# Kernel optimization log

Measured on AMD Instinct MI355X. Metric: run time of the kernel, lower is better.

The kernel has to match this reference:

```python
import jax, jax.numpy as jnp
import numpy as np

B, L, D, H, HD, FF, NL = 2, 2048, 1024, 16, 64, 4096, 2
EPS = 1e-5
NEG = -1e30


def setup_inputs() -> dict:
    key = jax.random.key(0)
    ks = jax.random.split(key, 20)
    x = jax.random.normal(ks[0], (B, L, D), jnp.float32)
    # RoPE tables, rotate-half convention: [L, HD]
    pos = jnp.arange(L, dtype=jnp.float32)
    freqs = 1.0 / (10000.0 ** (jnp.arange(0, HD, 2, dtype=jnp.float32) / HD))
    ang = pos[:, None] * freqs[None, :]              # [L, HD/2]
    cos = jnp.concatenate([jnp.cos(ang), jnp.cos(ang)], -1)
    sin = jnp.concatenate([jnp.sin(ang), jnp.sin(ang)], -1)
    s = 0.02
    wq = jax.random.normal(ks[1], (NL, D, D), jnp.float32) * s
    wk = jax.random.normal(ks[2], (NL, D, D), jnp.float32) * s
    wv = jax.random.normal(ks[3], (NL, D, D), jnp.float32) * s
    wo = jax.random.normal(ks[4], (NL, D, D), jnp.float32) * s
    w1 = jax.random.normal(ks[5], (NL, D, FF), jnp.float32) * s
    w2 = jax.random.normal(ks[6], (NL, FF, D), jnp.float32) * s
    w3 = jax.random.normal(ks[7], (NL, D, FF), jnp.float32) * s
    attn_norm = jnp.ones((NL, D), jnp.float32)
    mlp_norm = jnp.ones((NL, D), jnp.float32)
    final_norm = jnp.ones((D,), jnp.float32)
    rw1 = jax.random.normal(ks[8], (D, D), jnp.float32) * s
    rb1 = jnp.zeros((D,), jnp.float32)
    rw2 = jax.random.normal(ks[9], (D, 1), jnp.float32) * s
    rb2 = jnp.zeros((1,), jnp.float32)
    return dict(x=x, cos=cos, sin=sin, wq=wq, wk=wk, wv=wv, wo=wo,
                w1=w1, w2=w2, w3=w3, attn_norm=attn_norm, mlp_norm=mlp_norm,
                final_norm=final_norm, rw1=rw1, rb1=rb1, rw2=rw2, rb2=rb2)


def _rms(x, w):
    return x * jax.lax.rsqrt(jnp.mean(x * x, -1, keepdims=True) + EPS) * w


def _rope(t, cos, sin):
    # t: [B, L, H, HD]; cos/sin: [L, HD]
    t1, t2 = jnp.split(t, 2, axis=-1)
    rot = jnp.concatenate([-t2, t1], -1)
    return t * cos[None, :, None, :] + rot * sin[None, :, None, :]


def reference(x, cos, sin, wq, wk, wv, wo, w1, w2, w3,
              attn_norm, mlp_norm, final_norm, rw1, rb1, rw2, rb2):
    causal = jnp.tril(jnp.ones((L, L), bool))
    h = x
    for i in range(NL):  # small fixed layer loop
        a = _rms(h, attn_norm[i])
        q = _rope((a @ wq[i]).reshape(B, L, H, HD), cos, sin)
        k = _rope((a @ wk[i]).reshape(B, L, H, HD), cos, sin)
        v = (a @ wv[i]).reshape(B, L, H, HD)
        sc = jnp.einsum('bqhd,bkhd->bhqk', q, k) / np.float32(np.sqrt(HD))
        sc = jnp.where(causal, sc, NEG)
        o = jnp.einsum('bhqk,bkhd->bqhd', jax.nn.softmax(sc, -1), v)
        h = h + o.reshape(B, L, D) @ wo[i]
        m = _rms(h, mlp_norm[i])
        h = h + (jax.nn.silu(m @ w1[i]) * (m @ w3[i])) @ w2[i]
    h = _rms(h, final_norm)

    # router chunking: straight-through hard boundaries
    logits = (jax.nn.silu(h @ rw1 + rb1) @ rw2 + rb2)[..., 0]   # [B, L]
    probs = jax.nn.sigmoid(logits)
    hard = (probs > 0.5).astype(h.dtype)
    mask = probs + jax.lax.stop_gradient(hard - probs)
    mask = mask.at[:, 0].set(1.0)
    mhard = jax.lax.stop_gradient(mask)
    # select matrix: S padded to static upper bound L (rows >= counts are zero)
    cums = jnp.cumsum(mhard, -1)                                # [B, L]
    seg = jnp.arange(1, L + 1, dtype=cums.dtype)[None, :, None] # [1, S, 1]
    assignment = (cums[:, None, :] == seg).astype(h.dtype)      # [B, S, L]
    select = assignment * mask[:, None, :]
    compressed = jnp.einsum('bsl,bld->bsd', select, h)          # [B, S, D]
    boundary_positions = jnp.argsort(-mhard, axis=-1)           # stable in jax
    counts = mhard.sum(-1).astype(jnp.int32)
    avg_chunk_size = jnp.float32(L) / jnp.mean(counts.astype(jnp.float32))
    return (h, compressed, boundary_positions, counts, avg_chunk_size)
```

## Files before the change

### kernel.cpp

```cpp
#include <hip/hip_runtime.h>
#include <cmath>

#define B_  2
#define L_  2048
#define D_  1024
#define H_  16
#define FF_ 4096
#define NL_ 2
#define NT_ (B_*L_)
#define ND_ (NT_*D_)

typedef __attribute__((ext_vector_type(8))) short bf16x8;
typedef __attribute__((ext_vector_type(4))) float f32x4;

__device__ __forceinline__ short f2bf(float x){
  unsigned u = __builtin_bit_cast(unsigned, x);
  unsigned r = (u + 0x7fffu + ((u>>16)&1u)) >> 16;
  return (short)r;
}
__device__ __forceinline__ float bf2f(short s){
  unsigned u = ((unsigned)(unsigned short)s) << 16;
  return __builtin_bit_cast(float, u);
}
#define MFMA16(a,b,c) __builtin_amdgcn_mfma_f32_16x16x32_bf16(a,b,c,0,0,0)

__device__ __forceinline__ void gload16(const short* g, short* l){
  __builtin_amdgcn_global_load_lds((const __attribute__((address_space(1))) void*)g,
                                   (__attribute__((address_space(3))) void*)l, 16, 0, 0);
}

template<bool WF32>
__global__ __launch_bounds__(256) void k_rmsnorm_s(const float* __restrict__ in,
                                                   const float* __restrict__ w,
                                                   short* __restrict__ oh,
                                                   short* __restrict__ ol,
                                                   float* __restrict__ of){
  int row = blockIdx.x; int tid = threadIdx.x;
  float4 xv = ((const float4*)(in + (size_t)row*D_))[tid];
  float ss = xv.x*xv.x + xv.y*xv.y + xv.z*xv.z + xv.w*xv.w;
  #pragma unroll
  for (int off=32; off; off>>=1) ss += __shfl_xor(ss, off);
  __shared__ float wsum[4];
  if ((tid&63)==0) wsum[tid>>6] = ss;
  __syncthreads();
  float tot = wsum[0]+wsum[1]+wsum[2]+wsum[3];
  float scale = 1.0f / sqrtf(tot*(1.0f/(float)D_) + 1e-5f);
  float4 w4 = ((const float4*)w)[tid];
  float v[4] = {xv.x*scale*w4.x, xv.y*scale*w4.y, xv.z*scale*w4.z, xv.w*scale*w4.w};
  short4 hh, ll;
  short h0=f2bf(v[0]); hh.x=h0; ll.x=f2bf(v[0]-bf2f(h0));
  short h1=f2bf(v[1]); hh.y=h1; ll.y=f2bf(v[1]-bf2f(h1));
  short h2=f2bf(v[2]); hh.z=h2; ll.z=f2bf(v[2]-bf2f(h2));
  short h3=f2bf(v[3]); hh.w=h3; ll.w=f2bf(v[3]-bf2f(h3));
  *(short4*)(oh + (size_t)row*D_ + tid*4) = hh;
  *(short4*)(ol + (size_t)row*D_ + tid*4) = ll;
  if (WF32){
    float4 ov; ov.x=v[0]; ov.y=v[1]; ov.z=v[2]; ov.w=v[3];
    ((float4*)(of + (size_t)row*D_))[tid] = ov;
  }
}

__global__ __launch_bounds__(256) void k_wsplit(const float* __restrict__ src,
                                                short* __restrict__ dh,
                                                short* __restrict__ dl,
                                                int srcN, int kOff, int nOff, int KT){
  __shared__ float t[64][68];
  int k0 = blockIdx.x*64, n0v = blockIdx.y*64;
  int tid = threadIdx.x;
  #pragma unroll
  for (int p=0;p<4;p++){
    int r = p*16 + (tid>>4);
    int c4 = (tid&15)*4;
    float4 v = *(const float4*)(src + (size_t)(kOff + k0 + r)*srcN + nOff + n0v + c4);
    *(float4*)&t[r][c4] = v;
  }
  __syncthreads();
  int n = tid>>2, kk = (tid&3)*16;
  bf16x8 H0, L0, H1, L1;
  #pragma unroll
  for (int q=0;q<8;q++){
    float v = t[kk+q][n]; short h=f2bf(v); H0[q]=h; L0[q]=f2bf(v-bf2f(h));
  }
  #pragma unroll
  for (int q=0;q<8;q++){
    float v = t[kk+8+q][n]; short h=f2bf(v); H1[q]=h; L1[q]=f2bf(v-bf2f(h));
  }
  size_t dof = (size_t)(n0v + n)*KT + k0 + kk;
  *(bf16x8*)(dh + dof) = H0;  *(bf16x8*)(dh + dof + 8) = H1;
  *(bf16x8*)(dl + dof) = L0;  *(bf16x8*)(dl + dof + 8) = L1;
}

__global__ __launch_bounds__(256,2) void k_qkv_mm(const short* __restrict__ Ah,
                                                  const short* __restrict__ Al,
                                                  const short* __restrict__ Wh,
                                                  const short* __restrict__ Wl,
                                                  short* __restrict__ OutH){
  __shared__ short lds[32768];
  int tid = threadIdx.x, wid = tid>>6, lane = tid&63;
  int l15 = lane&15, l4 = lane>>4;
  int wr = wid>>1, wc = wid&1;
  int m0 = blockIdx.y*128, n0 = blockIdx.x*128;
  const int K = 1024;
  f32x4 acc[4][4];
  #pragma unroll
  for (int i=0;i<4;i++){
    #pragma unroll
    for (int j=0;j<4;j++) acc[i][j] = (f32x4){0.f,0.f,0.f,0.f};
  }
  const short* gsrc = (wid==0)?Ah:(wid==1)?Al:(wid==2)?Wh:Wl;
  int rb = (wid<2)? m0 : n0;
  int gcol = ((lane&7)^(lane>>3))*8;
  short* ldsw = lds + wid*8192;
  const short* gp0 = gsrc + (size_t)(rb + (lane>>3))*K + gcol;
  for (int k0=0; k0<K; k0+=64){
    const short* gp = gp0 + k0;
    #pragma unroll
    for (int lc=0; lc<16; ++lc)
      gload16(gp + (size_t)lc*8*K, ldsw + lc*512);
    __syncthreads();
    #pragma unroll
    for (int ks=0; ks<2; ++ks){
      bf16x8 af[4], alf[4], wf[4], wlf[4];
      int gs = ((ks*4 + l4) ^ (lane&7))*8;
      #pragma unroll
      for (int f=0; f<4; ++f){
        int ar = (wr*64 + f*16 + l15)*64 + gs;
        af[f]  = *(const bf16x8*)&lds[ar];
        alf[f] = *(const bf16x8*)&lds[8192 + ar];
        int wr2 = (wc*64 + f*16 + l15)*64 + gs;
        wf[f]  = *(const bf16x8*)&lds[16384 + wr2];
        wlf[f] = *(const bf16x8*)&lds[24576 + wr2];
      }
      #pragma unroll
      for (int i=0;i<4;i++){
        #pragma unroll
        for (int j=0;j<4;j++){
          acc[i][j] = MFMA16(af[i],  wf[j],  acc[i][j]);
          acc[i][j] = MFMA16(alf[i], wf[j],  acc[i][j]);
          acc[i][j] = MFMA16(af[i],  wlf[j], acc[i][j]);
        }
      }
    }
    __syncthreads();
  }
  int sel = n0 >> 10;
  short* oh = OutH + (size_t)sel*8388608;
  short* ol = oh + 4194304;
  int cb = (n0 & 1023) + wc*64;
  #pragma unroll
  for (int i=0;i<4;i++){
    #pragma unroll
    for (int j=0;j<4;j++){
      #pragma unroll
      for (int r=0;r<4;r++){
        size_t mg = (size_t)(m0 + wr*64 + i*16 + l4*4 + r);
        int ng = cb + j*16 + l15;
        float v = acc[i][j][r];
        short h = f2bf(v);
        oh[mg*1024 + ng] = h;
        ol[mg*1024 + ng] = f2bf(v - bf2f(h));
      }
    }
  }
}

template<int EPI>
__global__ __launch_bounds__(256,2) void k_mm64(const short* __restrict__ Ah,
                                                const short* __restrict__ Al,
                                                const short* __restrict__ Wh,
                                                const short* __restrict__ Wl,
                                                const short* __restrict__ W3h,
                                                const short* __restrict__ W3l,
                                                int K,
                                                float* __restrict__ Cf,
                                                const float* __restrict__ bias,
                                                short* __restrict__ Gh,
                                                short* __restrict__ Gl,
                                                int ldc){
  __shared__ short lds[(EPI==3)?32768:24576];
  int tid = threadIdx.x, wid = tid>>6, lane = tid&63;
  int l15 = lane&15, l4 = lane>>4;
  int m0 = blockIdx.y*128, n0 = blockIdx.x*64;
  f32x4 a1[2][4], a3[2][4];
  #pragma unroll
  for (int i=0;i<2;i++){
    #pragma unroll
    for (int j=0;j<4;j++){ a1[i][j]=(f32x4){0.f,0.f,0.f,0.f}; a3[i][j]=(f32x4){0.f,0.f,0.f,0.f}; }
  }
  int gcol = ((lane&7)^(lane>>3))*8;
  int l8 = lane>>3;
  const int NCH = (EPI==3)? 16 : 12;
  for (int k0=0; k0<K; k0+=64){
    for (int t=0; t<NCH; ++t){
      int c = wid*NCH + t;
      const short* sb; int row0; short* db;
      if (c < 32){
        sb = (c<16)? Ah : Al; row0 = m0 + (c&15)*8;
        db = lds + ((c<16)?0:8192) + (c&15)*512;
      } else {
        int wseg = (c-32)>>3;
        sb = (wseg==0)?Wh:(wseg==1)?Wl:(wseg==2)?W3h:W3l;
        row0 = n0 + (c&7)*8;
        db = lds + 16384 + wseg*4096 + (c&7)*512;
      }
      gload16(sb + (size_t)(row0 + l8)*K + k0 + gcol, db);
    }
    __syncthreads();
    #pragma unroll
    for (int ks=0; ks<2; ++ks){
      int gs = ((ks*4 + l4) ^ (lane&7))*8;
      bf16x8 af[2], alf[2], wh[4], wl[4];
      #pragma unroll
      for (int f=0; f<2; ++f){
        int ar = (wid*32 + f*16 + l15)*64 + gs;
        af[f]  = *(const bf16x8*)&lds[ar];
        alf[f] = *(const bf16x8*)&lds[8192 + ar];
      }
      #pragma unroll
      for (int f=0; f<4; ++f){
        int wr2 = (f*16 + l15)*64 + gs;
        wh[f] = *(const bf16x8*)&lds[16384 + wr2];
        wl[f] = *(const bf16x8*)&lds[20480 + wr2];
      }
      #pragma unroll
      for (int i=0;i<2;i++){
        #pragma unroll
        for (int j=0;j<4;j++){
          a1[i][j] = MFMA16(af[i],  wh[j], a1[i][j]);
          a1[i][j] = MFMA16(alf[i], wh[j], a1[i][j]);
          a1[i][j] = MFMA16(af[i],  wl[j], a1[i][j]);
        }
      }
      if (EPI==3){
        bf16x8 w3h[4], w3l[4];
        #pragma unroll
        for (int f=0; f<4; ++f){
          int wr2 = (f*16 + l15)*64 + gs;
          w3h[f] = *(const bf16x8*)&lds[24576 + wr2];
          w3l[f] = *(const bf16x8*)&lds[28672 + wr2];
        }
        #pragma unroll
        for (int i=0;i<2;i++){
          #pragma unroll
          for (int j=0;j<4;j++){
            a3[i][j] = MFMA16(af[i],  w3h[j], a3[i][j]);
            a3[i][j] = MFMA16(alf[i], w3h[j], a3[i][j]);
            a3[i][j] = MFMA16(af[i],  w3l[j], a3[i][j]);
          }
        }
      }
    }
    __syncthreads();
  }
  #pragma unroll
  for (int i=0;i<2;i++){
    #pragma unroll
    for (int j=0;j<4;j++){
      #pragma unroll
      for (int r=0;r<4;r++){
        size_t mg = (size_t)(m0 + wid*32 + i*16 + l4*4 + r);
        int ng = n0 + j*16 + l15;
        float v = a1[i][j][r];
        if (EPI==1){
          float* cp = Cf + mg*ldc + ng;
          *cp = *cp + v;
        } else if (EPI==2){
          float x = v + bias[ng];
          Cf[mg*ldc + ng] = x/(1.f+expf(-x));
        } else {
          float g = v/(1.f+expf(-v)) * a3[i][j][r];
          short h = f2bf(g);
          Gh[mg*2048 + ng] = h;
          Gl[mg*2048 + ng] = f2bf(g - bf2f(h));
        }
      }
    }
  }
}

__global__ __launch_bounds__(256) void k_prep_k(const short* __restrict__ kh,
                                                const short* __restrict__ kl,
                                                const float* __restrict__ cosT,
                                                const float* __restrict__ sinT,
                                                short* __restrict__ kf){
  int wave = threadIdx.x>>6, lane = threadIdx.x&63;
  int t16 = blockIdx.x*4 + wave;
  int bh = blockIdx.y; int b = bh>>4, h = bh&15;
  int l15 = lane&15, l4 = lane>>4;
  int tok = t16*16 + l15;
  const short* khp = kh + (size_t)(b*L_+tok)*D_ + h*64;
  const short* klp = kl + (size_t)(b*L_+tok)*D_ + h*64;
  int d0 = l4*8;
  bf16x8 ka  = *(const bf16x8*)(khp + d0);
  bf16x8 kb2 = *(const bf16x8*)(khp + 32 + d0);
  bf16x8 kla = *(const bf16x8*)(klp + d0);
  bf16x8 klb = *(const bf16x8*)(klp + 32 + d0);
  const float* cr = cosT + (size_t)tok*64;
  const float* sr = sinT + (size_t)tok*64;
  float c0[8], s0[8], c1[8], s1[8];
  *(float4*)&c0[0] = *(const float4*)(cr + d0);      *(float4*)&c0[4] = *(const float4*)(cr + d0 + 4);
  *(float4*)&c1[0] = *(const float4*)(cr + 32 + d0); *(float4*)&c1[4] = *(const float4*)(cr + 32 + d0 + 4);
  *(float4*)&s0[0] = *(const float4*)(sr + d0);      *(float4*)&s0[4] = *(const float4*)(sr + d0 + 4);
  *(float4*)&s1[0] = *(const float4*)(sr + 32 + d0); *(float4*)&s1[4] = *(const float4*)(sr + 32 + d0 + 4);
  bf16x8 h0, lo0, h1, lo1;
  #pragma unroll
  for (int j=0;j<8;j++){
    float k0v = bf2f(ka[j]) + bf2f(kla[j]);
    float k1v = bf2f(kb2[j]) + bf2f(klb[j]);
    float r0 = k0v*c0[j] - k1v*s0[j];
    float r1 = k1v*c1[j] + k0v*s1[j];
    short a = f2bf(r0); h0[j]=a; lo0[j]=f2bf(r0 - bf2f(a));
    short bS = f2bf(r1); h1[j]=bS; lo1[j]=f2bf(r1 - bf2f(bS));
  }
  size_t base = ((size_t)(bh*128 + t16)*4)*512 + lane*8;
  *(bf16x8*)(kf + base)        = h0;
  *(bf16x8*)(kf + base + 512)  = lo0;
  *(bf16x8*)(kf + base + 1024) = h1;
  *(bf16x8*)(kf + base + 1536) = lo1;
}

__global__ __launch_bounds__(256) void k_prep_v(const short* __restrict__ vh,
                                                const short* __restrict__ vl,
                                                short* __restrict__ vf){
  int wave = threadIdx.x>>6, lane = threadIdx.x&63;
  int kc = blockIdx.x;
  int bh = blockIdx.y; int b = bh>>4, h = bh&15;
  int dt = wave;
  int l15 = lane&15, l4 = lane>>4;
  bf16x8 hi, lo;
  #pragma unroll
  for (int i=0;i<8;i++){
    size_t off = (size_t)(b*L_ + kc*32 + l4*8 + i)*D_ + h*64 + dt*16 + l15;
    hi[i] = vh[off];
    lo[i] = vl[off];
  }
  size_t base = (((size_t)(bh*64 + kc)*4 + dt)*2)*512 + lane*8;
  *(bf16x8*)(vf + base)       = hi;
  *(bf16x8*)(vf + base + 512) = lo;
}

__global__ __launch_bounds__(256) void k_attn_mfma(const short* __restrict__ qhb,
                                                   const short* __restrict__ qlb,
                                                   const short* __restrict__ kf,
                                                   const short* __restrict__ vf,
                                                   const float* __restrict__ cosT,
                                                   const float* __restrict__ sinT,
                                                   short* __restrict__ oh,
                                                   short* __restrict__ ol){
  int qt = 31 - (int)blockIdx.x;
  int bh = blockIdx.y; int b = bh>>4, h = bh&15;
  int wave = threadIdx.x>>6, lane = threadIdx.x&63;
  int l15 = lane&15, l4 = lane>>4;
  __shared__ short pblob[4][2048];
  short* pb = pblob[wave];

  int tok = qt*64 + wave*16 + l15;
  const short* qhp = qhb + (size_t)(b*L_+tok)*D_ + h*64;
  const short* qlp = qlb + (size_t)(b*L_+tok)*D_ + h*64;
  int d0 = l4*8;
  bf16x8 qa  = *(const bf16x8*)(qhp + d0);
  bf16x8 qb2 = *(const bf16x8*)(qhp + 32 + d0);
  bf16x8 qla = *(const bf16x8*)(qlp + d0);
  bf16x8 qlb2= *(const bf16x8*)(qlp + 32 + d0);
  const float* cr = cosT + (size_t)tok*64;
  const float* sr = sinT + (size_t)tok*64;
  float c0[8], s0[8], c1[8], s1[8];
  *(float4*)&c0[0] = *(const float4*)(cr + d0);      *(float4*)&c0[4] = *(const float4*)(cr + d0 + 4);
  *(float4*)&c1[0] = *(const float4*)(cr + 32 + d0); *(float4*)&c1[4] = *(const float4*)(cr + 32 + d0 + 4);
  *(float4*)&s0[0] = *(const float4*)(sr + d0);      *(float4*)&s0[4] = *(const float4*)(sr + d0 + 4);
  *(float4*)&s1[0] = *(const float4*)(sr + 32 + d0); *(float4*)&s1[4] = *(const float4*)(sr + 32 + d0 + 4);
  bf16x8 qh0, ql0, qh1, ql1;
  #pragma unroll
  for (int j=0;j<8;j++){
    float q0v = bf2f(qa[j]) + bf2f(qla[j]);
    float q1v = bf2f(qb2[j]) + bf2f(qlb2[j]);
    float r0 = (q0v*c0[j] - q1v*s0[j]) * 0.125f;
    float r1 = (q1v*c1[j] + q0v*s1[j]) * 0.125f;
    short a = f2bf(r0); qh0[j]=a; ql0[j]=f2bf(r0 - bf2f(a));
    short bS = f2bf(r1); qh1[j]=bS; ql1[j]=f2bf(r1 - bf2f(bS));
  }

  f32x4 O[4];
  #pragma unroll
  for (int dt=0;dt<4;dt++) O[dt] = (f32x4){0.f,0.f,0.f,0.f};
  float m_[4] = {-1e30f,-1e30f,-1e30f,-1e30f};
  float ls[4] = {0.f,0.f,0.f,0.f};

  for (int kt=0; kt<=qt; ++kt){
    bool dtile = (kt == qt);
    f32x4 sr4[4];
    const short* kbase = kf + ((size_t)(bh*128 + kt*4)*4)*512 + lane*8;
    #pragma unroll
    for (int g=0; g<4; g++){
      f32x4 acc = (f32x4){0.f,0.f,0.f,0.f};
      if (!(dtile && g > wave)){
        const short* kp = kbase + (size_t)g*2048;
        bf16x8 kh0 = *(const bf16x8*)(kp);
        bf16x8 kl0 = *(const bf16x8*)(kp + 512);
        bf16x8 kh1 = *(const bf16x8*)(kp + 1024);
        bf16x8 kl1 = *(const bf16x8*)(kp + 1536);
        acc = MFMA16(qh0, kh0, acc); acc = MFMA16(qh1, kh1, acc);
        acc = MFMA16(ql0, kh0, acc); acc = MFMA16(ql1, kh1, acc);
        acc = MFMA16(qh0, kl0, acc); acc = MFMA16(qh1, kl1, acc);
      }
      sr4[g] = acc;
    }
    float p_[4][4];
    #pragma unroll
    for (int r=0; r<4; r++){
      int rowrel = wave*16 + l4*4 + r;
      float mx = -1e30f;
      float sv[4];
      #pragma unroll
      for (int g=0; g<4; g++){
        float v = sr4[g][r];
        if (dtile && (g*16 + l15) > rowrel) v = -1e30f;
        sv[g] = v; mx = fmaxf(mx, v);
      }
      #pragma unroll
      for (int off=1; off<16; off<<=1) mx = fmaxf(mx, __shfl_xor(mx, off));
      float nm = fmaxf(m_[r], mx);
      float al = __expf(m_[r] - nm);
      m_[r] = nm;
      float ps = 0.f;
      #pragma unroll
      for (int g=0; g<4; g++){ float pv = __expf(sv[g] - nm); p_[g][r] = pv; ps += pv; }
      #pragma unroll
      for (int off=1; off<16; off<<=1) ps += __shfl_xor(ps, off);
      ls[r] = ls[r]*al + ps;
      #pragma unroll
      for (int dt=0; dt<4; dt++) O[dt][r] *= al;
    }
    #pragma unroll
    for (int g=0; g<4; g++){
      int key = g*16 + l15;
      int cc = key>>5, sub = (key>>3)&3, ii = key&7;
      #pragma unroll
      for (int r=0; r<4; r++){
        float pv = p_[g][r];
        short ph = f2bf(pv);
        short pl = f2bf(pv - bf2f(ph));
        int idx = cc*1024 + (sub*16 + l4*4 + r)*8 + ii;
        pb[idx] = ph;
        pb[idx + 512] = pl;
      }
    }
    asm volatile("s_waitcnt lgkmcnt(0)" ::: "memory");
    const short* vbase = vf + ((size_t)(bh*64 + kt*2)*8)*512 + lane*8;
    #pragma unroll
    for (int cc=0; cc<2; cc++){
      bf16x8 pah = *(const bf16x8*)(pb + cc*1024 + lane*8);
      bf16x8 pal = *(const bf16x8*)(pb + cc*1024 + 512 + lane*8);
      #pragma unroll
      for (int dt=0; dt<4; dt++){
        const short* vp = vbase + (size_t)cc*4096 + dt*1024;
        bf16x8 vh = *(const bf16x8*)(vp);
        bf16x8 vl = *(const bf16x8*)(vp + 512);
        O[dt] = MFMA16(pah, vh, O[dt]);
        O[dt] = MFMA16(pal, vh, O[dt]);
        O[dt] = MFMA16(pah, vl, O[dt]);
      }
    }
  }
  #pragma unroll
  for (int r=0; r<4; r++){
    float inv = 1.0f / ls[r];
    size_t row = (size_t)(b*L_ + qt*64 + wave*16 + l4*4 + r);
    #pragma unroll
    for (int dt=0; dt<4; dt++){
      float v = O[dt][r]*inv;
      short hh = f2bf(v);
      oh[row*D_ + h*64 + dt*16 + l15] = hh;
      ol[row*D_ + h*64 + dt*16 + l15] = f2bf(v - bf2f(hh));
    }
  }
}

__global__ __launch_bounds__(256) void k_gemv(const float* __restrict__ T,
                                              const float* __restrict__ rw2,
                                              const float* __restrict__ rb2,
                                              float* __restrict__ logits){
  int row = blockIdx.x; int tid = threadIdx.x;
  float4 tv = ((const float4*)(T + (size_t)row*D_))[tid];
  float4 wv = ((const float4*)rw2)[tid];
  float s = tv.x*wv.x + tv.y*wv.y + tv.z*wv.z + tv.w*wv.w;
  #pragma unroll
  for (int off=32; off; off>>=1) s += __shfl_xor(s, off);
  __shared__ float ps[4];
  if ((tid&63)==0) ps[tid>>6] = s;
  __syncthreads();
  if (tid==0) logits[row] = ps[0]+ps[1]+ps[2]+ps[3] + rb2[0];
}

__global__ __launch_bounds__(256) void k_boundary(const float* __restrict__ logits,
                                                  float* __restrict__ pos_out,
                                                  int* __restrict__ hard,
                                                  int* __restrict__ cums,
                                                  int* __restrict__ counts){
  int b = blockIdx.x; int tid = threadIdx.x;
  __shared__ int part[256];
  int loc[8]; int s=0;
  int base = b*L_;
  #pragma unroll
  for (int j=0;j<8;j++){
    int ll = tid*8 + j;
    float lg = logits[base+ll];
    int hv = (ll==0) ? 1 : ((lg > 0.0f) ? 1 : 0);
    loc[j]=hv; s+=hv;
  }
  part[tid]=s; __syncthreads();
  for (int off=1; off<256; off<<=1){
    int v = part[tid];
    int add = (tid>=off) ? part[tid-off] : 0;
    __syncthreads();
    part[tid] = v + add;
    __syncthreads();
  }
  int total = part[255];
  int run = part[tid] - s;
  #pragma unroll
  for (int j=0;j<8;j++){
    int ll = tid*8+j;
    run += loc[j];
    hard[base+ll] = loc[j];
    cums[base+ll] = run;
    int idx = loc[j] ? (run-1) : (total + ll - run);
    pos_out[base+idx] = (float)ll;
  }
  if (tid==0) counts[b] = total;
}

__global__ __launch_bounds__(256) void k_scatter(const float* __restrict__ hf,
                                                 const int* __restrict__ hard,
                                                 const int* __restrict__ cums,
                                                 float* __restrict__ comp){
  int rowid = blockIdx.x;
  if (!hard[rowid]) return;
  int b = rowid >> 11;
  int s = cums[rowid]-1;
  const float4* src = (const float4*)(hf + (size_t)rowid*D_);
  float4* dst = (float4*)(comp + (size_t)(b*L_ + s)*D_);
  dst[threadIdx.x] = src[threadIdx.x];
}

__global__ void k_finalize(const int* __restrict__ counts, float* __restrict__ out){
  if (threadIdx.x==0 && blockIdx.x==0){
    float c0 = (float)counts[0], c1 = (float)counts[1];
    out[0]=c0; out[1]=c1;
    out[2] = (float)L_ / (0.5f*(c0+c1));
  }
}

extern "C" void kernel_launch(void* const* d_in, const int* in_sizes, int n_in,
                              void* d_out, int out_size, void* d_ws, size_t ws_size,
                              hipStream_t stream){
  const float* x      = (const float*)d_in[0];
  const float* cosT   = (const float*)d_in[1];
  const float* sinT   = (const float*)d_in[2];
  const float* wq     = (const float*)d_in[3];
  const float* wk     = (const float*)d_in[4];
  const float* wv     = (const float*)d_in[5];
  const float* wo     = (const float*)d_in[6];
  const float* w1     = (const float*)d_in[7];
  const float* w2     = (const float*)d_in[8];
  const float* w3     = (const float*)d_in[9];
  const float* attn_n = (const float*)d_in[10];
  const float* mlp_n  = (const float*)d_in[11];
  const float* final_n= (const float*)d_in[12];
  const float* rw1    = (const float*)d_in[13];
  const float* rb1    = (const float*)d_in[14];
  const float* rw2    = (const float*)d_in[15];
  const float* rb2    = (const float*)d_in[16];

  float* outF = (float*)d_out;
  float* hD   = outF;
  float* compD= outF + (size_t)ND_;
  float* posD = outF + (size_t)2*ND_;

  char* WS = (char*)d_ws;
  auto S = [&](size_t mb){ return (short*)(WS + mb*1048576ull); };
  auto F = [&](size_t mb){ return (float*)(WS + mb*1048576ull); };
  short *ah=S(0), *al=S(8);
  short *qh=S(16), *ql=S(24), *kh=S(32), *kl=S(40), *vh=S(48), *vl=S(56);
  short *qkvwt_h=S(64), *qkvwt_l=S(70);
  short *vf=S(64);
  short *kf=S(48);
  short *wot_h=S(32), *wot_l=S(34);
  short *gh=S(16), *gl=S(32);
  short *w1t_h=S(48), *w1t_l=S(52), *w3t_h=S(56), *w3t_l=S(60);
  short *w2t_h=S(64), *w2t_l=S(68);
  short *rw1t_h=S(16), *rw1t_l=S(18);
  float *ra=F(20);
  float *logits=F(76);
  int *hard=(int*)(logits+NT_), *cums=hard+NT_, *cnts=cums+NT_;
  short *oh=(short*)compD, *ol=oh+4194304;

  hipMemcpyAsync(hD, x, (size_t)ND_*sizeof(float), hipMemcpyDeviceToDevice, stream);

  for (int i=0;i<NL_;++i){
    k_rmsnorm_s<false><<<NT_,256,0,stream>>>(hD, attn_n + (size_t)i*D_, ah, al, nullptr);
    k_wsplit<<<dim3(16,16),256,0,stream>>>(wq + (size_t)i*D_*D_, qkvwt_h,         qkvwt_l,         1024, 0, 0, 1024);
    k_wsplit<<<dim3(16,16),256,0,stream>>>(wk + (size_t)i*D_*D_, qkvwt_h+1048576, qkvwt_l+1048576, 1024, 0, 0, 1024);
    k_wsplit<<<dim3(16,16),256,0,stream>>>(wv + (size_t)i*D_*D_, qkvwt_h+2097152, qkvwt_l+2097152, 1024, 0, 0, 1024);
    k_qkv_mm<<<dim3(24,32),256,0,stream>>>(ah, al, qkvwt_h, qkvwt_l, qh);
    k_prep_v<<<dim3(64,32),256,0,stream>>>(vh, vl, vf);
    k_prep_k<<<dim3(32,32),256,0,stream>>>(kh, kl, cosT, sinT, kf);
    k_wsplit<<<dim3(16,16),256,0,stream>>>(wo + (size_t)i*D_*D_, wot_h, wot_l, 1024, 0, 0, 1024);
    k_attn_mfma<<<dim3(32,32),256,0,stream>>>(qh, ql, kf, vf, cosT, sinT, oh, ol);
    k_mm64<1><<<dim3(16,32),256,0,stream>>>(oh, ol, wot_h, wot_l, nullptr, nullptr,
                                            1024, hD, nullptr, nullptr, nullptr, 1024);
    k_rmsnorm_s<false><<<NT_,256,0,stream>>>(hD, mlp_n + (size_t)i*D_, ah, al, nullptr);
    for (int hc=0; hc<2; ++hc){
      k_wsplit<<<dim3(16,32),256,0,stream>>>(w1 + (size_t)i*D_*FF_, w1t_h, w1t_l, 4096, 0, hc*2048, 1024);
      k_wsplit<<<dim3(16,32),256,0,stream>>>(w3 + (size_t)i*D_*FF_, w3t_h, w3t_l, 4096, 0, hc*2048, 1024);
      k_wsplit<<<dim3(32,16),256,0,stream>>>(w2 + (size_t)i*FF_*D_, w2t_h, w2t_l, 1024, hc*2048, 0, 2048);
      k_mm64<3><<<dim3(32,32),256,0,stream>>>(ah, al, w1t_h, w1t_l, w3t_h, w3t_l,
                                              1024, nullptr, nullptr, gh, gl, 0);
      k_mm64<1><<<dim3(16,32),256,0,stream>>>(gh, gl, w2t_h, w2t_l, nullptr, nullptr,
                                              2048, hD, nullptr, nullptr, nullptr, 1024);
    }
  }
  k_rmsnorm_s<true><<<NT_,256,0,stream>>>(hD, final_n, ah, al, hD);
  k_wsplit<<<dim3(16,16),256,0,stream>>>(rw1, rw1t_h, rw1t_l, 1024, 0, 0, 1024);
  k_mm64<2><<<dim3(16,32),256,0,stream>>>(ah, al, rw1t_h, rw1t_l, nullptr, nullptr,
                                          1024, ra, rb1, nullptr, nullptr, 1024);
  k_gemv<<<NT_,256,0,stream>>>(ra, rw2, rb2, logits);
  k_boundary<<<B_,256,0,stream>>>(logits, posD, hard, cums, cnts);
  hipMemsetAsync(compD, 0, (size_t)ND_*sizeof(float), stream);
  k_scatter<<<NT_,256,0,stream>>>(hD, hard, cums, compD);
  k_finalize<<<1,64,0,stream>>>(cnts, posD + NT_);
}
```

Measured before the change: 1.494 ms.

## Double-buffer GEMM and attention LDS staging, pair causal query tiles per block

The QKV and generic GEMM kernels now use two shared-memory buffers with 32-wide K steps. The next tile's async loads are issued before computing the current one, with explicit vmcnt waits and raw barriers, and wave priority is raised around the MFMA bursts. The attention kernel now stages K/V tiles through double-buffered LDS instead of reading them straight from global memory. Each block processes two complementary causal query tiles (31-p and p) to balance work, with the block index remapped across 512 blocks. This aims to hide global-load latency and even out causal load imbalance, at the cost of doubled LDS use, which may cut occupancy, and fragile hand-coded waitcnt counts.

```diff
diff --git a/kernel.cpp b/kernel.cpp
--- a/kernel.cpp
+++ b/kernel.cpp
@@ -95,7 +95,7 @@
                                                   const short* __restrict__ Wh,
                                                   const short* __restrict__ Wl,
                                                   short* __restrict__ OutH){
-  __shared__ short lds[32768];
+  __shared__ short sb2[2][16384];
   int tid = threadIdx.x, wid = tid>>6, lane = tid&63;
   int l15 = lane&15, l4 = lane>>4;
   int wr = wid>>1, wc = wid&1;
@@ -107,46 +107,54 @@
     #pragma unroll
     for (int j=0;j<4;j++) acc[i][j] = (f32x4){0.f,0.f,0.f,0.f};
   }
-  const short* gsrc = (wid==0)?Ah:(wid==1)?Al:(wid==2)?Wh:Wl;
+  const short* src = (wid==0)?Ah:(wid==1)?Al:(wid==2)?Wh:Wl;
   int rb = (wid<2)? m0 : n0;
-  int gcol = ((lane&7)^(lane>>3))*8;
-  short* ldsw = lds + wid*8192;
-  const short* gp0 = gsrc + (size_t)(rb + (lane>>3))*K + gcol;
-  for (int k0=0; k0<K; k0+=64){
-    const short* gp = gp0 + k0;
-    #pragma unroll
-    for (int lc=0; lc<16; ++lc)
-      gload16(gp + (size_t)lc*8*K, ldsw + lc*512);
-    __syncthreads();
-    #pragma unroll
-    for (int ks=0; ks<2; ++ks){
-      bf16x8 af[4], alf[4], wf[4], wlf[4];
-      int gs = ((ks*4 + l4) ^ (lane&7))*8;
-      #pragma unroll
-      for (int f=0; f<4; ++f){
-        int ar = (wr*64 + f*16 + l15)*64 + gs;
-        af[f]  = *(const bf16x8*)&lds[ar];
-        alf[f] = *(const bf16x8*)&lds[8192 + ar];
-        int wr2 = (wc*64 + f*16 + l15)*64 + gs;
-        wf[f]  = *(const bf16x8*)&lds[16384 + wr2];
-        wlf[f] = *(const bf16x8*)&lds[24576 + wr2];
-      }
-      #pragma unroll
-      for (int i=0;i<4;i++){
-        #pragma unroll
-        for (int j=0;j<4;j++){
-          acc[i][j] = MFMA16(af[i],  wf[j],  acc[i][j]);
-          acc[i][j] = MFMA16(alf[i], wf[j],  acc[i][j]);
-          acc[i][j] = MFMA16(af[i],  wlf[j], acc[i][j]);
-        }
-      }
-    }
-    __syncthreads();
+  int r_loc = lane>>2;
+  int cgrp = (lane&3) ^ ((lane>>3)&3);
+  const short* gbase = src + (size_t)(rb + r_loc)*K + cgrp*8;
+  auto stage = [&](short* dst, int k0){
+    #pragma unroll
+    for (int c=0;c<8;c++)
+      gload16(gbase + (size_t)c*16*K + k0, dst + wid*4096 + c*512);
+  };
+  int swzo = ((l4 ^ (l15>>1))&3)*8;
+  stage(sb2[0], 0);
+  for (int s=0; s<32; ++s){
+    short* cb = sb2[s&1];
+    if (s<31){
+      stage(sb2[(s&1)^1], (s+1)*32);
+      asm volatile("s_waitcnt vmcnt(8)" ::: "memory");
+    } else {
+      asm volatile("s_waitcnt vmcnt(0)" ::: "memory");
+    }
+    __builtin_amdgcn_s_barrier();
+    bf16x8 af[4], alf[4], wf[4], wlf[4];
+    #pragma unroll
+    for (int f=0; f<4; ++f){
+      int ar = (wr*64 + f*16 + l15)*32 + swzo;
+      af[f]  = *(const bf16x8*)&cb[ar];
+      alf[f] = *(const bf16x8*)&cb[4096 + ar];
+      int wr2 = (wc*64 + f*16 + l15)*32 + swzo;
+      wf[f]  = *(const bf16x8*)&cb[8192 + wr2];
+      wlf[f] = *(const bf16x8*)&cb[12288 + wr2];
+    }
+    __builtin_amdgcn_s_setprio(1);
+    #pragma unroll
+    for (int i=0;i<4;i++){
+      #pragma unroll
+      for (int j=0;j<4;j++){
+        acc[i][j] = MFMA16(af[i],  wf[j],  acc[i][j]);
+        acc[i][j] = MFMA16(alf[i], wf[j],  acc[i][j]);
+        acc[i][j] = MFMA16(af[i],  wlf[j], acc[i][j]);
+      }
+    }
+    __builtin_amdgcn_s_setprio(0);
+    __builtin_amdgcn_s_barrier();
   }
   int sel = n0 >> 10;
   short* oh = OutH + (size_t)sel*8388608;
   short* ol = oh + 4194304;
-  int cb = (n0 & 1023) + wc*64;
+  int cb2 = (n0 & 1023) + wc*64;
   #pragma unroll
   for (int i=0;i<4;i++){
     #pragma unroll
@@ -154,7 +162,7 @@
       #pragma unroll
       for (int r=0;r<4;r++){
         size_t mg = (size_t)(m0 + wr*64 + i*16 + l4*4 + r);
-        int ng = cb + j*16 + l15;
+        int ng = cb2 + j*16 + l15;
         float v = acc[i][j][r];
         short h = f2bf(v);
         oh[mg*1024 + ng] = h;
@@ -177,80 +185,94 @@
                                                 short* __restrict__ Gh,
                                                 short* __restrict__ Gl,
                                                 int ldc){
-  __shared__ short lds[(EPI==3)?32768:24576];
+  __shared__ short sb2[2][(EPI==3)?16384:12288];
   int tid = threadIdx.x, wid = tid>>6, lane = tid&63;
   int l15 = lane&15, l4 = lane>>4;
   int m0 = blockIdx.y*128, n0 = blockIdx.x*64;
+  const int NCH = (EPI==3)? 8 : 6;
   f32x4 a1[2][4], a3[2][4];
   #pragma unroll
   for (int i=0;i<2;i++){
     #pragma unroll
     for (int j=0;j<4;j++){ a1[i][j]=(f32x4){0.f,0.f,0.f,0.f}; a3[i][j]=(f32x4){0.f,0.f,0.f,0.f}; }
   }
-  int gcol = ((lane&7)^(lane>>3))*8;
-  int l8 = lane>>3;
-  const int NCH = (EPI==3)? 16 : 12;
-  for (int k0=0; k0<K; k0+=64){
-    for (int t=0; t<NCH; ++t){
-      int c = wid*NCH + t;
-      const short* sb; int row0; short* db;
-      if (c < 32){
-        sb = (c<16)? Ah : Al; row0 = m0 + (c&15)*8;
-        db = lds + ((c<16)?0:8192) + (c&15)*512;
+  int r_loc = lane>>2;
+  int cgrp = (lane&3) ^ ((lane>>3)&3);
+  auto stage = [&](short* dst, int k0){
+    #pragma unroll
+    for (int c=0;c<NCH;c++){
+      int ch = wid*NCH + c;
+      const short* sbp; int rowb; int ldso;
+      if (ch < 16){
+        sbp = (ch<8)? Ah : Al; rowb = m0 + (ch&7)*16;
+        ldso = ((ch<8)?0:4096) + (ch&7)*512;
       } else {
-        int wseg = (c-32)>>3;
-        sb = (wseg==0)?Wh:(wseg==1)?Wl:(wseg==2)?W3h:W3l;
-        row0 = n0 + (c&7)*8;
-        db = lds + 16384 + wseg*4096 + (c&7)*512;
-      }
-      gload16(sb + (size_t)(row0 + l8)*K + k0 + gcol, db);
-    }
-    __syncthreads();
-    #pragma unroll
-    for (int ks=0; ks<2; ++ks){
-      int gs = ((ks*4 + l4) ^ (lane&7))*8;
-      bf16x8 af[2], alf[2], wh[4], wl[4];
-      #pragma unroll
-      for (int f=0; f<2; ++f){
-        int ar = (wid*32 + f*16 + l15)*64 + gs;
-        af[f]  = *(const bf16x8*)&lds[ar];
-        alf[f] = *(const bf16x8*)&lds[8192 + ar];
-      }
+        int w = (ch-16)>>2;
+        sbp = (w==0)?Wh:(w==1)?Wl:(w==2)?W3h:W3l;
+        rowb = n0 + (ch&3)*16;
+        ldso = 8192 + w*2048 + (ch&3)*512;
+      }
+      gload16(sbp + (size_t)(rowb + r_loc)*K + k0 + cgrp*8, dst + ldso);
+    }
+  };
+  int swzo = ((l4 ^ (l15>>1))&3)*8;
+  int NS = K >> 5;
+  stage(sb2[0], 0);
+  for (int s=0; s<NS; ++s){
+    short* cb = sb2[s&1];
+    if (s < NS-1){
+      stage(sb2[(s&1)^1], (s+1)*32);
+      if (EPI==3) asm volatile("s_waitcnt vmcnt(8)" ::: "memory");
+      else        asm volatile("s_waitcnt vmcnt(6)" ::: "memory");
+    } else {
+      asm volatile("s_waitcnt vmcnt(0)" ::: "memory");
+    }
+    __builtin_amdgcn_s_barrier();
+    bf16x8 af[2], alf[2], whf[4], wlf[4];
+    #pragma unroll
+    for (int f=0; f<2; ++f){
+      int ar = (wid*32 + f*16 + l15)*32 + swzo;
+      af[f]  = *(const bf16x8*)&cb[ar];
+      alf[f] = *(const bf16x8*)&cb[4096 + ar];
+    }
+    #pragma unroll
+    for (int f=0; f<4; ++f){
+      int wr2 = (f*16 + l15)*32 + swzo;
+      whf[f] = *(const bf16x8*)&cb[8192 + wr2];
+      wlf[f] = *(const bf16x8*)&cb[10240 + wr2];
+    }
+    __builtin_amdgcn_s_setprio(1);
+    #pragma unroll
+    for (int i=0;i<2;i++){
+      #pragma unroll
+      for (int j=0;j<4;j++){
+        a1[i][j] = MFMA16(af[i],  whf[j], a1[i][j]);
+        a1[i][j] = MFMA16(alf[i], whf[j], a1[i][j]);
+        a1[i][j] = MFMA16(af[i],  wlf[j], a1[i][j]);
+      }
+    }
+    __builtin_amdgcn_s_setprio(0);
+    if (EPI==3){
+      bf16x8 w3h[4], w3l[4];
       #pragma unroll
       for (int f=0; f<4; ++f){
-        int wr2 = (f*16 + l15)*64 + gs;
-        wh[f] = *(const bf16x8*)&lds[16384 + wr2];
-        wl[f] = *(const bf16x8*)&lds[20480 + wr2];
-      }
+        int wr2 = (f*16 + l15)*32 + swzo;
+        w3h[f] = *(const bf16x8*)&cb[12288 + wr2];
+        w3l[f] = *(const bf16x8*)&cb[14336 + wr2];
+      }
+      __builtin_amdgcn_s_setprio(1);
       #pragma unroll
       for (int i=0;i<2;i++){
         #pragma unroll
         for (int j=0;j<4;j++){
-          a1[i][j] = MFMA16(af[i],  wh[j], a1[i][j]);
-          a1[i][j] = MFMA16(alf[i], wh[j], a1[i][j]);
-          a1[i][j] = MFMA16(af[i],  wl[j], a1[i][j]);
+          a3[i][j] = MFMA16(af[i],  w3h[j], a3[i][j]);
+          a3[i][j] = MFMA16(alf[i], w3h[j], a3[i][j]);
+          a3[i][j] = MFMA16(af[i],  w3l[j], a3[i][j]);
         }
       }
-      if (EPI==3){
-        bf16x8 w3h[4], w3l[4];
-        #pragma unroll
-        for (int f=0; f<4; ++f){
-          int wr2 = (f*16 + l15)*64 + gs;
-          w3h[f] = *(const bf16x8*)&lds[24576 + wr2];
-          w3l[f] = *(const bf16x8*)&lds[28672 + wr2];
-        }
-        #pragma unroll
-        for (int i=0;i<2;i++){
-          #pragma unroll
-          for (int j=0;j<4;j++){
-            a3[i][j] = MFMA16(af[i],  w3h[j], a3[i][j]);
-            a3[i][j] = MFMA16(alf[i], w3h[j], a3[i][j]);
-            a3[i][j] = MFMA16(af[i],  w3l[j], a3[i][j]);
-          }
-        }
-      }
-    }
-    __syncthreads();
+      __builtin_amdgcn_s_setprio(0);
+    }
+    __builtin_amdgcn_s_barrier();
   }
   #pragma unroll
   for (int i=0;i<2;i++){
@@ -347,131 +369,165 @@
                                                    const float* __restrict__ sinT,
                                                    short* __restrict__ oh,
                                                    short* __restrict__ ol){
-  int qt = 31 - (int)blockIdx.x;
-  int bh = blockIdx.y; int b = bh>>4, h = bh&15;
+  int bid = blockIdx.x;
+  int logical = (bid&7)*64 + (bid>>3);
+  int bh = logical>>4, pair = logical&15;
+  int b = bh>>4, h = bh&15;
   int wave = threadIdx.x>>6, lane = threadIdx.x&63;
   int l15 = lane&15, l4 = lane>>4;
+  __shared__ short kvs[2][16384];
   __shared__ short pblob[4][2048];
   short* pb = pblob[wave];
 
-  int tok = qt*64 + wave*16 + l15;
-  const short* qhp = qhb + (size_t)(b*L_+tok)*D_ + h*64;
-  const short* qlp = qlb + (size_t)(b*L_+tok)*D_ + h*64;
-  int d0 = l4*8;
-  bf16x8 qa  = *(const bf16x8*)(qhp + d0);
-  bf16x8 qb2 = *(const bf16x8*)(qhp + 32 + d0);
-  bf16x8 qla = *(const bf16x8*)(qlp + d0);
-  bf16x8 qlb2= *(const bf16x8*)(qlp + 32 + d0);
-  const float* cr = cosT + (size_t)tok*64;
-  const float* sr = sinT + (size_t)tok*64;
-  float c0[8], s0[8], c1[8], s1[8];
-  *(float4*)&c0[0] = *(const float4*)(cr + d0);      *(float4*)&c0[4] = *(const float4*)(cr + d0 + 4);
-  *(float4*)&c1[0] = *(const float4*)(cr + 32 + d0); *(float4*)&c1[4] = *(const float4*)(cr + 32 + d0 + 4);
-  *(float4*)&s0[0] = *(const float4*)(sr + d0);      *(float4*)&s0[4] = *(const float4*)(sr + d0 + 4);
-  *(float4*)&s1[0] = *(const float4*)(sr + 32 + d0); *(float4*)&s1[4] = *(const float4*)(sr + 32 + d0 + 4);
-  bf16x8 qh0, ql0, qh1, ql1;
-  #pragma unroll
-  for (int j=0;j<8;j++){
-    float q0v = bf2f(qa[j]) + bf2f(qla[j]);
-    float q1v = bf2f(qb2[j]) + bf2f(qlb2[j]);
-    float r0 = (q0v*c0[j] - q1v*s0[j]) * 0.125f;
-    float r1 = (q1v*c1[j] + q0v*s1[j]) * 0.125f;
-    short a = f2bf(r0); qh0[j]=a; ql0[j]=f2bf(r0 - bf2f(a));
-    short bS = f2bf(r1); qh1[j]=bS; ql1[j]=f2bf(r1 - bf2f(bS));
-  }
-
-  f32x4 O[4];
-  #pragma unroll
-  for (int dt=0;dt<4;dt++) O[dt] = (f32x4){0.f,0.f,0.f,0.f};
-  float m_[4] = {-1e30f,-1e30f,-1e30f,-1e30f};
-  float ls[4] = {0.f,0.f,0.f,0.f};
-
-  for (int kt=0; kt<=qt; ++kt){
-    bool dtile = (kt == qt);
-    f32x4 sr4[4];
-    const short* kbase = kf + ((size_t)(bh*128 + kt*4)*4)*512 + lane*8;
-    #pragma unroll
-    for (int g=0; g<4; g++){
-      f32x4 acc = (f32x4){0.f,0.f,0.f,0.f};
-      if (!(dtile && g > wave)){
-        const short* kp = kbase + (size_t)g*2048;
-        bf16x8 kh0 = *(const bf16x8*)(kp);
-        bf16x8 kl0 = *(const bf16x8*)(kp + 512);
-        bf16x8 kh1 = *(const bf16x8*)(kp + 1024);
-        bf16x8 kl1 = *(const bf16x8*)(kp + 1536);
-        acc = MFMA16(qh0, kh0, acc); acc = MFMA16(qh1, kh1, acc);
-        acc = MFMA16(ql0, kh0, acc); acc = MFMA16(ql1, kh1, acc);
-        acc = MFMA16(qh0, kl0, acc); acc = MFMA16(qh1, kl1, acc);
-      }
-      sr4[g] = acc;
-    }
-    float p_[4][4];
+  auto stage = [&](int bufi, int kt){
+    const short* kg = kf + ((size_t)(bh*128 + kt*4))*2048;
+    const short* vg = vf + ((size_t)(bh*64 + kt*2))*4096;
+    short* dst = kvs[bufi];
+    #pragma unroll
+    for (int c=0;c<8;c++){
+      int ch = wave*8 + c;
+      const short* src = (ch<16)? (kg + ch*512) : (vg + (ch-16)*512);
+      gload16(src + lane*8, dst + ch*512);
+    }
+  };
+
+  for (int half=0; half<2; ++half){
+    int qt = (half==0) ? (31-pair) : pair;
+    stage(0, 0);
+    int tok = qt*64 + wave*16 + l15;
+    const short* qhp = qhb + (size_t)(b*L_+tok)*D_ + h*64;
+    const short* qlp = qlb + (size_t)(b*L_+tok)*D_ + h*64;
+    int d0 = l4*8;
+    bf16x8 qa  = *(const bf16x8*)(qhp + d0);
+    bf16x8 qb2 = *(const bf16x8*)(qhp + 32 + d0);
+    bf16x8 qla = *(const bf16x8*)(qlp + d0);
+    bf16x8 qlb2= *(const bf16x8*)(qlp + 32 + d0);
+    const float* cr = cosT + (size_t)tok*64;
+    const float* sr = sinT + (size_t)tok*64;
+    float c0[8], s0[8], c1[8], s1[8];
+    *(float4*)&c0[0] = *(const float4*)(cr + d0);      *(float4*)&c0[4] = *(const float4*)(cr + d0 + 4);
+    *(float4*)&c1[0] = *(const float4*)(cr + 32 + d0); *(float4*)&c1[4] = *(const float4*)(cr + 32 + d0 + 4);
+    *(float4*)&s0[0] = *(const float4*)(sr + d0);      *(float4*)&s0[4] = *(const float4*)(sr + d0 + 4);
+    *(float4*)&s1[0] = *(const float4*)(sr + 32 + d0); *(float4*)&s1[4] = *(const float4*)(sr + 32 + d0 + 4);
+    bf16x8 qh0, ql0, qh1, ql1;
+    #pragma unroll
+    for (int j=0;j<8;j++){
+      float q0v = bf2f(qa[j]) + bf2f(qla[j]);
+      float q1v = bf2f(qb2[j]) + bf2f(qlb2[j]);
+      float r0 = (q0v*c0[j] - q1v*s0[j]) * 0.125f;
+      float r1 = (q1v*c1[j] + q0v*s1[j]) * 0.125f;
+      short a = f2bf(r0); qh0[j]=a; ql0[j]=f2bf(r0 - bf2f(a));
+      short bS = f2bf(r1); qh1[j]=bS; ql1[j]=f2bf(r1 - bf2f(bS));
+    }
+
+    f32x4 O[4];
+    #pragma unroll
+    for (int dt=0;dt<4;dt++) O[dt] = (f32x4){0.f,0.f,0.f,0.f};
+    float m_[4] = {-1e30f,-1e30f,-1e30f,-1e30f};
+    float ls[4] = {0.f,0.f,0.f,0.f};
+
+    int cur = 0;
+    for (int kt=0; kt<=qt; ++kt){
+      bool haveNext = (kt < qt);
+      if (haveNext){
+        stage(cur^1, kt+1);
+        asm volatile("s_waitcnt vmcnt(8)" ::: "memory");
+      } else {
+        asm volatile("s_waitcnt vmcnt(0)" ::: "memory");
+      }
+      __builtin_amdgcn_s_barrier();
+      const short* Kl = kvs[cur];
+      const short* Vl = kvs[cur] + 8192;
+      bool dtile = (kt == qt);
+      f32x4 sr4[4];
+      #pragma unroll
+      for (int g=0; g<4; g++){
+        f32x4 acc = (f32x4){0.f,0.f,0.f,0.f};
+        if (!(dtile && g > wave)){
+          const short* kp = Kl + g*2048 + lane*8;
+          bf16x8 kh0 = *(const bf16x8*)(kp);
+          bf16x8 kl0 = *(const bf16x8*)(kp + 512);
+          bf16x8 kh1 = *(const bf16x8*)(kp + 1024);
+          bf16x8 kl1 = *(const bf16x8*)(kp + 1536);
+          __builtin_amdgcn_s_setprio(1);
+          acc = MFMA16(qh0, kh0, acc); acc = MFMA16(qh1, kh1, acc);
+          acc = MFMA16(ql0, kh0, acc); acc = MFMA16(ql1, kh1, acc);
+          acc = MFMA16(qh0, kl0, acc); acc = MFMA16(qh1, kl1, acc);
+          __builtin_amdgcn_s_setprio(0);
+        }
+        sr4[g] = acc;
+      }
+      float p_[4][4];
+      #pragma unroll
+      for (int r=0; r<4; r++){
+        int rowrel = wave*16 + l4*4 + r;
+        float mx = -1e30f;
+        float sv[4];
+        #pragma unroll
+        for (int g=0; g<4; g++){
+          float v = sr4[g][r];
+          if (dtile && (g*16 + l15) > rowrel) v = -1e30f;
+          sv[g] = v; mx = fmaxf(mx, v);
+        }
+        #pragma unroll
+        for (int off=1; off<16; off<<=1) mx = fmaxf(mx, __shfl_xor(mx, off));
+        float nm = fmaxf(m_[r], mx);
+        float al = __expf(m_[r] - nm);
+        m_[r] = nm;
+        float ps = 0.f;
+        #pragma unroll
+        for (int g=0; g<4; g++){ float pv = __expf(sv[g] - nm); p_[g][r] = pv; ps += pv; }
+        #pragma unroll
+        for (int off=1; off<16; off<<=1) ps += __shfl_xor(ps, off);
+        ls[r] = ls[r]*al + ps;
+        #pragma unroll
+        for (int dt=0; dt<4; dt++) O[dt][r] *= al;
+      }
+      #pragma unroll
+      for (int g=0; g<4; g++){
+        int key = g*16 + l15;
+        int cc = key>>5, sub = (key>>3)&3, ii = key&7;
+        #pragma unroll
+        for (int r=0; r<4; r++){
+          float pv = p_[g][r];
+          short ph = f2bf(pv);
+          short pl = f2bf(pv - bf2f(ph));
+          int idx = cc*1024 + (sub*16 + l4*4 + r)*8 + ii;
+          pb[idx] = ph;
+          pb[idx + 512] = pl;
+        }
+      }
+      asm volatile("s_waitcnt lgkmcnt(0)" ::: "memory");
+      #pragma unroll
+      for (int cc=0; cc<2; cc++){
+        bf16x8 pah = *(const bf16x8*)(pb + cc*1024 + lane*8);
+        bf16x8 pal = *(const bf16x8*)(pb + cc*1024 + 512 + lane*8);
+        const short* vp = Vl + cc*4096 + lane*8;
+        __builtin_amdgcn_s_setprio(1);
+        #pragma unroll
+        for (int dt=0; dt<4; dt++){
+          bf16x8 vh = *(const bf16x8*)(vp + dt*1024);
+          bf16x8 vl = *(const bf16x8*)(vp + dt*1024 + 512);
+          O[dt] = MFMA16(pah, vh, O[dt]);
+          O[dt] = MFMA16(pal, vh, O[dt]);
+          O[dt] = MFMA16(pah, vl, O[dt]);
+        }
+        __builtin_amdgcn_s_setprio(0);
+      }
+      __builtin_amdgcn_s_barrier();
+      cur ^= 1;
+    }
     #pragma unroll
     for (int r=0; r<4; r++){
-      int rowrel = wave*16 + l4*4 + r;
-      float mx = -1e30f;
-      float sv[4];
-      #pragma unroll
-      for (int g=0; g<4; g++){
-        float v = sr4[g][r];
-        if (dtile && (g*16 + l15) > rowrel) v = -1e30f;
-        sv[g] = v; mx = fmaxf(mx, v);
-      }
-      #pragma unroll
-      for (int off=1; off<16; off<<=1) mx = fmaxf(mx, __shfl_xor(mx, off));
-      float nm = fmaxf(m_[r], mx);
-      float al = __expf(m_[r] - nm);
-      m_[r] = nm;
-      float ps = 0.f;
-      #pragma unroll
-      for (int g=0; g<4; g++){ float pv = __expf(sv[g] - nm); p_[g][r] = pv; ps += pv; }
-      #pragma unroll
-      for (int off=1; off<16; off<<=1) ps += __shfl_xor(ps, off);
-      ls[r] = ls[r]*al + ps;
-      #pragma unroll
-      for (int dt=0; dt<4; dt++) O[dt][r] *= al;
-    }
-    #pragma unroll
-    for (int g=0; g<4; g++){
-      int key = g*16 + l15;
-      int cc = key>>5, sub = (key>>3)&3, ii = key&7;
-      #pragma unroll
-      for (int r=0; r<4; r++){
-        float pv = p_[g][r];
-        short ph = f2bf(pv);
-        short pl = f2bf(pv - bf2f(ph));
-        int idx = cc*1024 + (sub*16 + l4*4 + r)*8 + ii;
-        pb[idx] = ph;
-        pb[idx + 512] = pl;
-      }
-    }
-    asm volatile("s_waitcnt lgkmcnt(0)" ::: "memory");
-    const short* vbase = vf + ((size_t)(bh*64 + kt*2)*8)*512 + lane*8;
-    #pragma unroll
-    for (int cc=0; cc<2; cc++){
-      bf16x8 pah = *(const bf16x8*)(pb + cc*1024 + lane*8);
-      bf16x8 pal = *(const bf16x8*)(pb + cc*1024 + 512 + lane*8);
+      float inv = 1.0f / ls[r];
+      size_t row = (size_t)(b*L_ + qt*64 + wave*16 + l4*4 + r);
       #pragma unroll
       for (int dt=0; dt<4; dt++){
-        const short* vp = vbase + (size_t)cc*4096 + dt*1024;
-        bf16x8 vh = *(const bf16x8*)(vp);
-        bf16x8 vl = *(const bf16x8*)(vp + 512);
-        O[dt] = MFMA16(pah, vh, O[dt]);
-        O[dt] = MFMA16(pal, vh, O[dt]);
-        O[dt] = MFMA16(pah, vl, O[dt]);
-      }
-    }
-  }
-  #pragma unroll
-  for (int r=0; r<4; r++){
-    float inv = 1.0f / ls[r];
-    size_t row = (size_t)(b*L_ + qt*64 + wave*16 + l4*4 + r);
-    #pragma unroll
-    for (int dt=0; dt<4; dt++){
-      float v = O[dt][r]*inv;
-      short hh = f2bf(v);
-      oh[row*D_ + h*64 + dt*16 + l15] = hh;
-      ol[row*D_ + h*64 + dt*16 + l15] = f2bf(v - bf2f(hh));
+        float v = O[dt][r]*inv;
+        short hh = f2bf(v);
+        oh[row*D_ + h*64 + dt*16 + l15] = hh;
+        ol[row*D_ + h*64 + dt*16 + l15] = f2bf(v - bf2f(hh));
+      }
     }
   }
 }
@@ -606,7 +662,7 @@
     k_prep_v<<<dim3(64,32),256,0,stream>>>(vh, vl, vf);
     k_prep_k<<<dim3(32,32),256,0,stream>>>(kh, kl, cosT, sinT, kf);
     k_wsplit<<<dim3(16,16),256,0,stream>>>(wo + (size_t)i*D_*D_, wot_h, wot_l, 1024, 0, 0, 1024);
-    k_attn_mfma<<<dim3(32,32),256,0,stream>>>(qh, ql, kf, vf, cosT, sinT, oh, ol);
+    k_attn_mfma<<<dim3(512),256,0,stream>>>(qh, ql, kf, vf, cosT, sinT, oh, ol);
     k_mm64<1><<<dim3(16,32),256,0,stream>>>(oh, ol, wot_h, wot_l, nullptr, nullptr,
                                             1024, hD, nullptr, nullptr, nullptr, 1024);
     k_rmsnorm_s<false><<<NT_,256,0,stream>>>(hD, mlp_n + (size_t)i*D_, ah, al, nullptr);
```

Result: slower. 2.295 ms (+53.6%).
